# Optimization experiments

Hardware: AMD Instinct MI355X
Metric: run time of the kernel (lower is better)

## Reference

```python
import jax, jax.numpy as jnp
import numpy as np

D_MODEL = 1024
NUM_HEADS = 16
D_K = D_MODEL // NUM_HEADS
SCALE = float(np.sqrt(D_K))


def setup_inputs() -> dict:
    key = jax.random.key(0)
    ks = jax.random.split(key, 12)
    B, S = 4, 2048
    s = 1.0 / np.sqrt(D_MODEL)
    inp = {
        'query': jax.random.normal(ks[0], (B, S, D_MODEL), jnp.float32),
        'key':   jax.random.normal(ks[1], (B, S, D_MODEL), jnp.float32),
        'value': jax.random.normal(ks[2], (B, S, D_MODEL), jnp.float32),
        'Wq': jax.random.normal(ks[3], (D_MODEL, D_MODEL), jnp.float32) * s,
        'bq': jax.random.normal(ks[4], (D_MODEL,), jnp.float32) * s,
        'Wk': jax.random.normal(ks[5], (D_MODEL, D_MODEL), jnp.float32) * s,
        'bk': jax.random.normal(ks[6], (D_MODEL,), jnp.float32) * s,
        'Wv': jax.random.normal(ks[7], (D_MODEL, D_MODEL), jnp.float32) * s,
        'bv': jax.random.normal(ks[8], (D_MODEL,), jnp.float32) * s,
        'Wo': jax.random.normal(ks[9], (D_MODEL, D_MODEL), jnp.float32) * s,
        'bo': jax.random.normal(ks[10], (D_MODEL,), jnp.float32) * s,
    }
    return inp


def reference(query, key, value, Wq, bq, Wk, bk, Wv, bv, Wo, bo):
    B, Sq, _ = query.shape
    Skv = key.shape[1]
    # torch Linear: x @ W.T + b
    def proj(x, W, b, S):
        y = jnp.einsum('bsd,ed->bse', x, W) + b
        return y.reshape(B, S, NUM_HEADS, D_K).transpose(0, 2, 1, 3)  # [B,H,S,dk]
    Q = proj(query, Wq, bq, Sq)
    K = proj(key, Wk, bk, Skv)
    V = proj(value, Wv, bv, Skv)
    scores = jnp.einsum('bhqd,bhkd->bhqk', Q, K) / SCALE  # [B,H,Sq,Skv]
    attn = jax.nn.softmax(scores, axis=-1)  # dropout=0 -> identity
    out = jnp.einsum('bhqk,bhkd->bhqd', attn, V)
    out = out.transpose(0, 2, 1, 3).reshape(B, Sq, D_MODEL)
    out = jnp.einsum('bsd,ed->bse', out, Wo) + bo
    return out
```

## Files before the change

kernel.cpp:

```cpp
#include <hip/hip_runtime.h>


typedef __attribute__((ext_vector_type(8))) __bf16 bf16x8;
typedef __attribute__((ext_vector_type(4))) __bf16 bf16x4;
typedef __attribute__((ext_vector_type(4))) float f32x4;

#define SCALE_FOLD 0.18033688011112043f

__device__ __forceinline__ void async_copy16(const void* g, void* lds) {
  __builtin_amdgcn_global_load_lds(
      (const __attribute__((address_space(1))) void*)g,
      (__attribute__((address_space(3))) void*)lds, 16, 0, 0);
}

template <int ROWS>
__device__ __forceinline__ void stage_tile(const __bf16* __restrict__ g, int ld,
                                           __bf16* lds, int tid) {
  const int wave_base = tid & ~63;
#pragma unroll
  for (int r = 0; r < ROWS / 32; ++r) {
    int slot = r * 256 + tid;
    int row = slot >> 3;
    int c = slot & 7;
    int gc = c ^ (row & 7);
    async_copy16(g + row * ld + gc * 8, lds + (r * 256 + wave_base) * 8);
  }
}

__device__ __forceinline__ bf16x8 frag_ld(const __bf16* lds, int row, int chunk) {
  return *(const bf16x8*)(lds + row * 64 + ((chunk ^ (row & 7)) << 3));
}

__global__ void cvt_bf16(const float* __restrict__ src, __bf16* __restrict__ dst,
                         int n4) {
  int i = blockIdx.x * blockDim.x + threadIdx.x;
  if (i < n4) {
    float4 v = ((const float4*)src)[i];
    bf16x4 o = {(__bf16)v.x, (__bf16)v.y, (__bf16)v.z, (__bf16)v.w};
    ((bf16x4*)dst)[i] = o;
  }
}

__global__ __launch_bounds__(256) void gemm_bt(const __bf16* __restrict__ A,
                                               const __bf16* __restrict__ B,
                                               const float* __restrict__ bias,
                                               void* __restrict__ out, int K,
                                               int mode) {
  __shared__ alignas(16) __bf16 Alds[128 * 64];
  __shared__ alignas(16) __bf16 Blds[128 * 64];

  const int tid = threadIdx.x;
  const int lane = tid & 63;
  const int w = tid >> 6;
  const int wm = w >> 1, wn = w & 1;
  const int l15 = lane & 15, quad = lane >> 4;
  const int m0 = blockIdx.y * 128, n0 = blockIdx.x * 128;

  f32x4 acc[4][4] = {};

  for (int k0 = 0; k0 < K; k0 += 64) {
    stage_tile<128>(A + m0 * K + k0, K, Alds, tid);
    stage_tile<128>(B + n0 * K + k0, K, Blds, tid);
    __syncthreads();
#pragma unroll
    for (int kc = 0; kc < 2; ++kc) {
      bf16x8 af[4], bfr[4];
#pragma unroll
      for (int mi = 0; mi < 4; ++mi)
        af[mi] = frag_ld(Alds, wm * 64 + mi * 16 + l15, kc * 4 + quad);
#pragma unroll
      for (int ni = 0; ni < 4; ++ni)
        bfr[ni] = frag_ld(Blds, wn * 64 + ni * 16 + l15, kc * 4 + quad);
#pragma unroll
      for (int mi = 0; mi < 4; ++mi)
#pragma unroll
        for (int ni = 0; ni < 4; ++ni)
          acc[mi][ni] = __builtin_amdgcn_mfma_f32_16x16x32_bf16(
              af[mi], bfr[ni], acc[mi][ni], 0, 0, 0);
    }
    __syncthreads();
  }

#pragma unroll
  for (int mi = 0; mi < 4; ++mi) {
#pragma unroll
    for (int i = 0; i < 4; ++i) {
      int grow = m0 + wm * 64 + mi * 16 + quad * 4 + i;
#pragma unroll
      for (int ni = 0; ni < 4; ++ni) {
        int gcol = n0 + wn * 64 + ni * 16 + l15;
        float v = acc[mi][ni][i];
        if (mode == 3) {
          v += bias[gcol];
          ((float*)out)[grow * 1024 + gcol] = v;
        } else if (mode == 2) {
          v += bias[grow];
          int h = grow >> 6, dd = grow & 63;
          int b = gcol >> 11, s = gcol & 2047;
          ((__bf16*)out)[(((b * 16 + h) * 64 + dd) * 2048) + s] = (__bf16)v;
        } else {
          v += bias[gcol];
          if (mode == 0) v *= SCALE_FOLD;
          int h = gcol >> 6, dd = gcol & 63;
          int b = grow >> 11, s = grow & 2047;
          ((__bf16*)out)[(((b * 16 + h) * 2048 + s) * 64) + dd] = (__bf16)v;
        }
      }
    }
  }
}

__global__ __launch_bounds__(256) void attn_kernel(const __bf16* __restrict__ Qg,
                                                   const __bf16* __restrict__ Kg,
                                                   const __bf16* __restrict__ Vt,
                                                   __bf16* __restrict__ AO) {
  __shared__ alignas(16) __bf16 Klds[64 * 64];
  __shared__ alignas(16) __bf16 Vlds[64 * 64];
  __shared__ alignas(16) __bf16 PQ[128 * 64];

  const int tid = threadIdx.x;
  const int lane = tid & 63;
  const int w = tid >> 6;
  const int l15 = lane & 15, quad = lane >> 4;
  const int bh = blockIdx.y;
  const int q0 = blockIdx.x * 128;
  const int S = 2048;

  const __bf16* Qbase = Qg + (size_t)bh * S * 64;
  const __bf16* Kbase = Kg + (size_t)bh * S * 64;
  const __bf16* Vbase = Vt + (size_t)bh * 64 * S;

  stage_tile<128>(Qbase + q0 * 64, 64, PQ, tid);
  __syncthreads();
  bf16x8 qf[2][2];
#pragma unroll
  for (int qi = 0; qi < 2; ++qi)
#pragma unroll
    for (int kc = 0; kc < 2; ++kc)
      qf[qi][kc] = frag_ld(PQ, w * 32 + qi * 16 + l15, kc * 4 + quad);
  __syncthreads();

  const bf16x8 ones = {__bf16(1.f), __bf16(1.f), __bf16(1.f), __bf16(1.f),
                       __bf16(1.f), __bf16(1.f), __bf16(1.f), __bf16(1.f)};

  f32x4 oacc[2][4] = {};
  f32x4 lacc[2] = {};

  __bf16* Pw = PQ + w * 32 * 64;

  for (int kv0 = 0; kv0 < S; kv0 += 64) {
    stage_tile<64>(Kbase + kv0 * 64, 64, Klds, tid);
    stage_tile<64>(Vbase + kv0, S, Vlds, tid);
    __syncthreads();

    f32x4 sacc[4][2] = {};
#pragma unroll
    for (int kc = 0; kc < 2; ++kc) {
      bf16x8 kf[4];
#pragma unroll
      for (int ci = 0; ci < 4; ++ci)
        kf[ci] = frag_ld(Klds, ci * 16 + l15, kc * 4 + quad);
#pragma unroll
      for (int ci = 0; ci < 4; ++ci)
#pragma unroll
        for (int qi = 0; qi < 2; ++qi)
          sacc[ci][qi] = __builtin_amdgcn_mfma_f32_16x16x32_bf16(
              kf[ci], qf[qi][kc], sacc[ci][qi], 0, 0, 0);
    }

#pragma unroll
    for (int ci = 0; ci < 4; ++ci) {
#pragma unroll
      for (int qi = 0; qi < 2; ++qi) {
        bf16x4 pk;
#pragma unroll
        for (int i = 0; i < 4; ++i)
          pk[i] = (__bf16)__builtin_amdgcn_exp2f(sacc[ci][qi][i]);
        int qrow = qi * 16 + l15;
        int addr = qrow * 64 + (((2 * ci + (quad >> 1)) ^ (qrow & 7)) << 3) +
                   ((quad & 1) << 2);
        *(bf16x4*)(Pw + addr) = pk;
      }
    }

#pragma unroll
    for (int kc = 0; kc < 2; ++kc) {
      bf16x8 pf[2], vf[4];
#pragma unroll
      for (int mi = 0; mi < 2; ++mi)
        pf[mi] = frag_ld(Pw, mi * 16 + l15, kc * 4 + quad);
#pragma unroll
      for (int ni = 0; ni < 4; ++ni)
        vf[ni] = frag_ld(Vlds, ni * 16 + l15, kc * 4 + quad);
#pragma unroll
      for (int mi = 0; mi < 2; ++mi)
        lacc[mi] = __builtin_amdgcn_mfma_f32_16x16x32_bf16(pf[mi], ones,
                                                           lacc[mi], 0, 0, 0);
#pragma unroll
      for (int mi = 0; mi < 2; ++mi)
#pragma unroll
        for (int ni = 0; ni < 4; ++ni)
          oacc[mi][ni] = __builtin_amdgcn_mfma_f32_16x16x32_bf16(
              pf[mi], vf[ni], oacc[mi][ni], 0, 0, 0);
    }
    __syncthreads();
  }

  const int b = bh >> 4;
  const int hh = bh & 15;
#pragma unroll
  for (int mi = 0; mi < 2; ++mi) {
#pragma unroll
    for (int i = 0; i < 4; ++i) {
      int s = q0 + w * 32 + mi * 16 + quad * 4 + i;
      float inv_l = 1.f / lacc[mi][i];
#pragma unroll
      for (int ni = 0; ni < 4; ++ni) {
        int d = ni * 16 + l15;
        AO[((size_t)(b * 2048 + s)) * 1024 + hh * 64 + d] =
            (__bf16)(oacc[mi][ni][i] * inv_l);
      }
    }
  }
}

extern "C" void kernel_launch(void* const* d_in, const int* in_sizes, int n_in,
                              void* d_out, int out_size, void* d_ws,
                              size_t ws_size, hipStream_t stream) {
  const float* q_in = (const float*)d_in[0];
  const float* k_in = (const float*)d_in[1];
  const float* v_in = (const float*)d_in[2];
  const float* Wq = (const float*)d_in[3];
  const float* bq = (const float*)d_in[4];
  const float* Wk = (const float*)d_in[5];
  const float* bk = (const float*)d_in[6];
  const float* Wv = (const float*)d_in[7];
  const float* bv = (const float*)d_in[8];
  const float* Wo = (const float*)d_in[9];
  const float* bo = (const float*)d_in[10];

  const size_t SZ_X = (size_t)8192 * 1024 * 2;
  const size_t SZ_W = (size_t)1024 * 1024 * 2;
  char* p = (char*)d_ws;
  __bf16* xq = (__bf16*)p; p += SZ_X;
  __bf16* xk = (__bf16*)p; p += SZ_X;
  __bf16* xv = (__bf16*)p; p += SZ_X;
  __bf16* wqb = (__bf16*)p; p += SZ_W;
  __bf16* wkb = (__bf16*)p; p += SZ_W;
  __bf16* wvb = (__bf16*)p; p += SZ_W;
  __bf16* wob = (__bf16*)p; p += SZ_W;
  __bf16* Qb = (__bf16*)p; p += SZ_X;
  __bf16* Kb = (__bf16*)p; p += SZ_X;
  __bf16* Vtb = (__bf16*)p; p += SZ_X;
  __bf16* AOb = (__bf16*)p; p += SZ_X;

  const int nx4 = 8192 * 1024 / 4, nw4 = 1024 * 1024 / 4;
  cvt_bf16<<<nx4 / 256, 256, 0, stream>>>(q_in, xq, nx4);
  cvt_bf16<<<nx4 / 256, 256, 0, stream>>>(k_in, xk, nx4);
  cvt_bf16<<<nx4 / 256, 256, 0, stream>>>(v_in, xv, nx4);
  cvt_bf16<<<nw4 / 256, 256, 0, stream>>>(Wq, wqb, nw4);
  cvt_bf16<<<nw4 / 256, 256, 0, stream>>>(Wk, wkb, nw4);
  cvt_bf16<<<nw4 / 256, 256, 0, stream>>>(Wv, wvb, nw4);
  cvt_bf16<<<nw4 / 256, 256, 0, stream>>>(Wo, wob, nw4);

  gemm_bt<<<dim3(8, 64), 256, 0, stream>>>(xq, wqb, bq, Qb, 1024, 0);
  gemm_bt<<<dim3(8, 64), 256, 0, stream>>>(xk, wkb, bk, Kb, 1024, 1);
  gemm_bt<<<dim3(64, 8), 256, 0, stream>>>(wvb, xv, bv, Vtb, 1024, 2);

  attn_kernel<<<dim3(16, 64), 256, 0, stream>>>(Qb, Kb, Vtb, AOb);

  gemm_bt<<<dim3(8, 64), 256, 0, stream>>>(AOb, wob, bo, d_out, 1024, 3);
}
```

Before: 412.0 us.

## Double-buffer K/V in attention, widen query tile, and batch kernel launches

```diff
diff --git a/kernel.cpp b/kernel.cpp
--- a/kernel.cpp
+++ b/kernel.cpp
@@ -31,8 +31,11 @@
   return *(const bf16x8*)(lds + row * 64 + ((chunk ^ (row & 7)) << 3));
 }
 
-__global__ void cvt_bf16(const float* __restrict__ src, __bf16* __restrict__ dst,
-                         int n4) {
+__global__ void cvt3(const float* __restrict__ s0, const float* __restrict__ s1,
+                     const float* __restrict__ s2, __bf16* d0, __bf16* d1,
+                     __bf16* d2, int n4) {
+  const float* src = blockIdx.y == 0 ? s0 : (blockIdx.y == 1 ? s1 : s2);
+  __bf16* dst = blockIdx.y == 0 ? d0 : (blockIdx.y == 1 ? d1 : d2);
   int i = blockIdx.x * blockDim.x + threadIdx.x;
   if (i < n4) {
     float4 v = ((const float4*)src)[i];
@@ -41,20 +44,32 @@
   }
 }
 
-__global__ __launch_bounds__(256) void gemm_bt(const __bf16* __restrict__ A,
-                                               const __bf16* __restrict__ B,
-                                               const float* __restrict__ bias,
-                                               void* __restrict__ out, int K,
-                                               int mode) {
-  __shared__ alignas(16) __bf16 Alds[128 * 64];
-  __shared__ alignas(16) __bf16 Blds[128 * 64];
-
+__global__ void cvt4(const float* __restrict__ s0, const float* __restrict__ s1,
+                     const float* __restrict__ s2, const float* __restrict__ s3,
+                     __bf16* d0, __bf16* d1, __bf16* d2, __bf16* d3, int n4) {
+  const float* src = blockIdx.y == 0 ? s0
+                     : (blockIdx.y == 1 ? s1 : (blockIdx.y == 2 ? s2 : s3));
+  __bf16* dst =
+      blockIdx.y == 0 ? d0 : (blockIdx.y == 1 ? d1 : (blockIdx.y == 2 ? d2 : d3));
+  int i = blockIdx.x * blockDim.x + threadIdx.x;
+  if (i < n4) {
+    float4 v = ((const float4*)src)[i];
+    bf16x4 o = {(__bf16)v.x, (__bf16)v.y, (__bf16)v.z, (__bf16)v.w};
+    ((bf16x4*)dst)[i] = o;
+  }
+}
+
+__device__ __forceinline__ void gemm_body(const __bf16* __restrict__ A,
+                                          const __bf16* __restrict__ B,
+                                          const float* __restrict__ bias,
+                                          void* __restrict__ out, int K,
+                                          int mode, int m0, int n0,
+                                          __bf16* Alds, __bf16* Blds) {
   const int tid = threadIdx.x;
   const int lane = tid & 63;
   const int w = tid >> 6;
   const int wm = w >> 1, wn = w & 1;
   const int l15 = lane & 15, quad = lane >> 4;
-  const int m0 = blockIdx.y * 128, n0 = blockIdx.x * 128;
 
   f32x4 acc[4][4] = {};
 
@@ -110,60 +125,94 @@
   }
 }
 
-__global__ __launch_bounds__(256) void attn_kernel(const __bf16* __restrict__ Qg,
-                                                   const __bf16* __restrict__ Kg,
-                                                   const __bf16* __restrict__ Vt,
-                                                   __bf16* __restrict__ AO) {
-  __shared__ alignas(16) __bf16 Klds[64 * 64];
-  __shared__ alignas(16) __bf16 Vlds[64 * 64];
-  __shared__ alignas(16) __bf16 PQ[128 * 64];
+__global__ __launch_bounds__(256) void gemm_qkv(
+    const __bf16* __restrict__ xq, const __bf16* __restrict__ xk,
+    const __bf16* __restrict__ xv, const __bf16* __restrict__ wq,
+    const __bf16* __restrict__ wk, const __bf16* __restrict__ wv,
+    const float* __restrict__ bq, const float* __restrict__ bk,
+    const float* __restrict__ bv, __bf16* Qb, __bf16* Kb, __bf16* Vtb) {
+  __shared__ alignas(16) __bf16 Alds[128 * 64];
+  __shared__ alignas(16) __bf16 Blds[128 * 64];
+  const int z = blockIdx.z;
+  if (z == 0) {
+    gemm_body(xq, wq, bq, Qb, 1024, 0, blockIdx.y * 128, blockIdx.x * 128,
+              Alds, Blds);
+  } else if (z == 1) {
+    gemm_body(xk, wk, bk, Kb, 1024, 1, blockIdx.y * 128, blockIdx.x * 128,
+              Alds, Blds);
+  } else {
+    gemm_body(wv, xv, bv, Vtb, 1024, 2, blockIdx.x * 128, blockIdx.y * 128,
+              Alds, Blds);
+  }
+}
+
+__global__ __launch_bounds__(256) void gemm_out(const __bf16* __restrict__ A,
+                                                const __bf16* __restrict__ B,
+                                                const float* __restrict__ bias,
+                                                float* __restrict__ out) {
+  __shared__ alignas(16) __bf16 Alds[128 * 64];
+  __shared__ alignas(16) __bf16 Blds[128 * 64];
+  gemm_body(A, B, bias, out, 1024, 3, blockIdx.y * 128, blockIdx.x * 128, Alds,
+            Blds);
+}
+
+__global__ __launch_bounds__(256, 2) void attn_kernel(
+    const __bf16* __restrict__ Qg, const __bf16* __restrict__ Kg,
+    const __bf16* __restrict__ Vt, __bf16* __restrict__ AO) {
+  __shared__ alignas(16) __bf16 Klds[2][64 * 64];
+  __shared__ alignas(16) __bf16 Vlds[2][64 * 64];
+  __shared__ alignas(16) __bf16 PQ[256 * 64];
 
   const int tid = threadIdx.x;
   const int lane = tid & 63;
   const int w = tid >> 6;
   const int l15 = lane & 15, quad = lane >> 4;
   const int bh = blockIdx.y;
-  const int q0 = blockIdx.x * 128;
+  const int q0 = blockIdx.x * 256;
   const int S = 2048;
 
   const __bf16* Qbase = Qg + (size_t)bh * S * 64;
   const __bf16* Kbase = Kg + (size_t)bh * S * 64;
   const __bf16* Vbase = Vt + (size_t)bh * 64 * S;
 
-  stage_tile<128>(Qbase + q0 * 64, 64, PQ, tid);
+  stage_tile<256>(Qbase + q0 * 64, 64, PQ, tid);
+  stage_tile<64>(Kbase, 64, Klds[0], tid);
+  stage_tile<64>(Vbase, S, Vlds[0], tid);
   __syncthreads();
-  bf16x8 qf[2][2];
-#pragma unroll
-  for (int qi = 0; qi < 2; ++qi)
+  bf16x8 qf[4][2];
+#pragma unroll
+  for (int qi = 0; qi < 4; ++qi)
 #pragma unroll
     for (int kc = 0; kc < 2; ++kc)
-      qf[qi][kc] = frag_ld(PQ, w * 32 + qi * 16 + l15, kc * 4 + quad);
+      qf[qi][kc] = frag_ld(PQ, w * 64 + qi * 16 + l15, kc * 4 + quad);
   __syncthreads();
 
   const bf16x8 ones = {__bf16(1.f), __bf16(1.f), __bf16(1.f), __bf16(1.f),
                        __bf16(1.f), __bf16(1.f), __bf16(1.f), __bf16(1.f)};
 
-  f32x4 oacc[2][4] = {};
-  f32x4 lacc[2] = {};
-
-  __bf16* Pw = PQ + w * 32 * 64;
-
-  for (int kv0 = 0; kv0 < S; kv0 += 64) {
-    stage_tile<64>(Kbase + kv0 * 64, 64, Klds, tid);
-    stage_tile<64>(Vbase + kv0, S, Vlds, tid);
-    __syncthreads();
-
-    f32x4 sacc[4][2] = {};
+  f32x4 oacc[4][4] = {};
+  f32x4 lacc[4] = {};
+
+  __bf16* Pw = PQ + w * 64 * 64;
+
+  for (int t = 0; t < 32; ++t) {
+    const int cur = t & 1;
+    if (t + 1 < 32) {
+      stage_tile<64>(Kbase + (t + 1) * 64 * 64, 64, Klds[cur ^ 1], tid);
+      stage_tile<64>(Vbase + (t + 1) * 64, S, Vlds[cur ^ 1], tid);
+    }
+
+    f32x4 sacc[4][4] = {};
 #pragma unroll
     for (int kc = 0; kc < 2; ++kc) {
       bf16x8 kf[4];
 #pragma unroll
       for (int ci = 0; ci < 4; ++ci)
-        kf[ci] = frag_ld(Klds, ci * 16 + l15, kc * 4 + quad);
+        kf[ci] = frag_ld(Klds[cur], ci * 16 + l15, kc * 4 + quad);
 #pragma unroll
       for (int ci = 0; ci < 4; ++ci)
 #pragma unroll
-        for (int qi = 0; qi < 2; ++qi)
+        for (int qi = 0; qi < 4; ++qi)
           sacc[ci][qi] = __builtin_amdgcn_mfma_f32_16x16x32_bf16(
               kf[ci], qf[qi][kc], sacc[ci][qi], 0, 0, 0);
     }
@@ -171,7 +220,7 @@
 #pragma unroll
     for (int ci = 0; ci < 4; ++ci) {
 #pragma unroll
-      for (int qi = 0; qi < 2; ++qi) {
+      for (int qi = 0; qi < 4; ++qi) {
         bf16x4 pk;
 #pragma unroll
         for (int i = 0; i < 4; ++i)
@@ -185,19 +234,19 @@
 
 #pragma unroll
     for (int kc = 0; kc < 2; ++kc) {
-      bf16x8 pf[2], vf[4];
-#pragma unroll
-      for (int mi = 0; mi < 2; ++mi)
+      bf16x8 pf[4], vf[4];
+#pragma unroll
+      for (int mi = 0; mi < 4; ++mi)
         pf[mi] = frag_ld(Pw, mi * 16 + l15, kc * 4 + quad);
 #pragma unroll
       for (int ni = 0; ni < 4; ++ni)
-        vf[ni] = frag_ld(Vlds, ni * 16 + l15, kc * 4 + quad);
-#pragma unroll
-      for (int mi = 0; mi < 2; ++mi)
+        vf[ni] = frag_ld(Vlds[cur], ni * 16 + l15, kc * 4 + quad);
+#pragma unroll
+      for (int mi = 0; mi < 4; ++mi)
         lacc[mi] = __builtin_amdgcn_mfma_f32_16x16x32_bf16(pf[mi], ones,
                                                            lacc[mi], 0, 0, 0);
 #pragma unroll
-      for (int mi = 0; mi < 2; ++mi)
+      for (int mi = 0; mi < 4; ++mi)
 #pragma unroll
         for (int ni = 0; ni < 4; ++ni)
           oacc[mi][ni] = __builtin_amdgcn_mfma_f32_16x16x32_bf16(
@@ -209,10 +258,10 @@
   const int b = bh >> 4;
   const int hh = bh & 15;
 #pragma unroll
-  for (int mi = 0; mi < 2; ++mi) {
+  for (int mi = 0; mi < 4; ++mi) {
 #pragma unroll
     for (int i = 0; i < 4; ++i) {
-      int s = q0 + w * 32 + mi * 16 + quad * 4 + i;
+      int s = q0 + w * 64 + mi * 16 + quad * 4 + i;
       float inv_l = 1.f / lacc[mi][i];
 #pragma unroll
       for (int ni = 0; ni < 4; ++ni) {
@@ -255,19 +304,15 @@
   __bf16* AOb = (__bf16*)p; p += SZ_X;
 
   const int nx4 = 8192 * 1024 / 4, nw4 = 1024 * 1024 / 4;
-  cvt_bf16<<<nx4 / 256, 256, 0, stream>>>(q_in, xq, nx4);
-  cvt_bf16<<<nx4 / 256, 256, 0, stream>>>(k_in, xk, nx4);
-  cvt_bf16<<<nx4 / 256, 256, 0, stream>>>(v_in, xv, nx4);
-  cvt_bf16<<<nw4 / 256, 256, 0, stream>>>(Wq, wqb, nw4);
-  cvt_bf16<<<nw4 / 256, 256, 0, stream>>>(Wk, wkb, nw4);
-  cvt_bf16<<<nw4 / 256, 256, 0, stream>>>(Wv, wvb, nw4);
-  cvt_bf16<<<nw4 / 256, 256, 0, stream>>>(Wo, wob, nw4);
-
-  gemm_bt<<<dim3(8, 64), 256, 0, stream>>>(xq, wqb, bq, Qb, 1024, 0);
-  gemm_bt<<<dim3(8, 64), 256, 0, stream>>>(xk, wkb, bk, Kb, 1024, 1);
-  gemm_bt<<<dim3(64, 8), 256, 0, stream>>>(wvb, xv, bv, Vtb, 1024, 2);
-
-  attn_kernel<<<dim3(16, 64), 256, 0, stream>>>(Qb, Kb, Vtb, AOb);
-
-  gemm_bt<<<dim3(8, 64), 256, 0, stream>>>(AOb, wob, bo, d_out, 1024, 3);
-}
+  cvt3<<<dim3(nx4 / 256, 3), 256, 0, stream>>>(q_in, k_in, v_in, xq, xk, xv,
+                                               nx4);
+  cvt4<<<dim3(nw4 / 256, 4), 256, 0, stream>>>(Wq, Wk, Wv, Wo, wqb, wkb, wvb,
+                                               wob, nw4);
+
+  gemm_qkv<<<dim3(8, 64, 3), 256, 0, stream>>>(xq, xk, xv, wqb, wkb, wvb, bq,
+                                               bk, bv, Qb, Kb, Vtb);
+
+  attn_kernel<<<dim3(8, 64), 256, 0, stream>>>(Qb, Kb, Vtb, AOb);
+
+  gemm_out<<<dim3(8, 64), 256, 0, stream>>>(AOb, wob, bo, (float*)d_out);
+}
```

After: 345.8 us. -16.1%, faster.
